# Kernel tuning notes

Measured on AMD Instinct MI355X. Metric: run time of the kernel, lower is better.

## Reference

```python
import jax, jax.numpy as jnp
import numpy as np

# Dimensions (see shape_source): 192x192 images, 10 MC samples, 4 classes (3 fg), batch 16
B, S, CLS, H, W = 16, 10, 4, 192, 192
FG = CLS - 1
FSCALE = 3   # neighbor-count kernel
CSCALE = 3   # constraint-reward kernel
K = float(CSCALE * CSCALE)


def setup_inputs() -> dict:
    key = jax.random.key(0)
    k1, k2 = jax.random.split(key)
    logits = jax.random.normal(k1, (B, CLS, H, W), dtype=jnp.float32)
    preds = jax.nn.softmax(logits, axis=1)          # per-pixel class probabilities
    samples = jax.random.randint(k2, (B, S, H, W), 0, CLS, dtype=jnp.int32)  # sampled label maps
    return {"preds": preds, "samples": samples}


def _conv_ones(x, ksize):
    # x: [N, H, W]; all-ones ksize x ksize conv, SAME padding (== pad (k-1)/2 in torch)
    kern = jnp.ones((1, 1, ksize, ksize), x.dtype)
    y = jax.lax.conv_general_dilated(x[:, None], kern, (1, 1), 'SAME')
    return y[:, 0]


def _dilate8(m):
    # 3x3 max-pool == one step of 8-connectivity dilation (skimage full connectivity)
    return jax.lax.reduce_window(m, 0.0, jax.lax.max, (3, 3), (1, 1), 'SAME')


def _flood(fg, seed):
    # connected component of fg containing flat index `seed` (8-connectivity),
    # equivalent to skimage.flood_fill from the seed followed by == new_value
    m0 = jnp.zeros(fg.size, fg.dtype).at[seed].set(1.0).reshape(fg.shape) * fg
    def cond(st):
        return st[1]
    def body(st):
        m, _ = st
        d = _dilate8(m) * fg
        return d, jnp.any(d != m)
    m, _ = jax.lax.while_loop(cond, body, (m0, jnp.array(True)))
    return m


def _connectivity_rewards(samples):
    # samples: [B, S, H, W] int class maps -> rewards [B, S, H, W]
    cls_ids = jnp.arange(1, CLS)
    fg = (samples[:, :, None] == cls_ids[None, None, :, None, None]).astype(jnp.float32)  # [B,S,FG,H,W]
    fgf = fg.reshape(-1, H, W)                     # [B*S*FG, H, W]
    nb = _conv_ones(fgf, FSCALE) * fgf             # foreground neighbor counts
    seeds = jnp.argmax(nb.reshape(nb.shape[0], -1), axis=1)  # seed = max-neighbor pixel (first max)
    comp = jax.vmap(_flood)(fgf, seeds)            # largest-seeded connected component
    fc = _conv_ones(comp, CSCALE) * comp           # F_fg_neigbors
    reward = fc / K                                # soft reward
    per_c = reward - (fgf - comp)                  # + isolation penalty: -(fg - fill_connect)
    return per_c.reshape(B, S, FG, H, W).sum(axis=2)


def reference(preds, samples):
    rewards = _connectivity_rewards(samples)       # [B,S,H,W], constant wrt preds
    # prob of the sampled class at each pixel: preds[b, samples[b,s,h,w], h, w]
    probs = jnp.take_along_axis(
        jnp.broadcast_to(preds[:, None], (B, S, CLS, H, W)),
        samples[:, :, None].astype(jnp.int32), axis=2)[:, :, 0]
    # REINFORCE-style constraint loss: maximize reward-weighted log-prob
    loss = -(jnp.log(probs + 1e-8) * rewards).mean()
    return loss
```

## Files before the change

kernel.cpp:

```cpp
#include <hip/hip_runtime.h>
#include <stdint.h>

#define BB 16
#define SS 10
#define CLSN 4
#define FGN 3
#define HH 192
#define WW 192
#define NPIX (HH * WW)
#define WPR 3
#define NWORDS (HH * WPR)
#define NTHREADS 1024
#define NWAVES 16
#define CHUNK (NWORDS / NWAVES)

typedef unsigned long long u64;

#define FAD(a, b, c, s, cy)            \
    do {                               \
        u64 t_ = (a) ^ (b);            \
        (s) = t_ ^ (c);                \
        (cy) = ((a) & (b)) | (t_ & (c)); \
    } while (0)

#define SMEAR3(u0, u1, u2, s0, s1, s2)                          \
    do {                                                        \
        (s0) = (u0) | ((u0) << 1) | ((u0) >> 1) | ((u1) << 63); \
        (s1) = (u1) | ((u1) << 1) | ((u0) >> 63) | ((u1) >> 1) | ((u2) << 63); \
        (s2) = (u2) | ((u2) << 1) | ((u1) >> 63) | ((u2) >> 1); \
    } while (0)

__device__ __forceinline__ void plane9(const u64* bd, int k,
                                       u64& P0, u64& P1, u64& P2, u64& P3, u64& mid)
{
    const int r = k / WPR;
    const int wc = k - r * WPR;
    u64 rows[3][3];
#pragma unroll
    for (int di = 0; di < 3; ++di) {
        int rr = r + di - 1;
#pragma unroll
        for (int dj = 0; dj < 3; ++dj) {
            int ww = wc + dj - 1;
            rows[di][dj] = (rr >= 0 && rr < HH && ww >= 0 && ww < WPR)
                           ? bd[rr * WPR + ww] : 0ULL;
        }
    }
    mid = rows[1][1];
    u64 in[9];
#pragma unroll
    for (int i = 0; i < 3; ++i) {
        u64 m = rows[i][1], lf = rows[i][0], rg = rows[i][2];
        in[3 * i + 0] = m;
        in[3 * i + 1] = (m << 1) | (lf >> 63);
        in[3 * i + 2] = (m >> 1) | (rg << 63);
    }
    u64 s0a, c0a, s0b, c0b, s0c, c0c, c0d, s1a, c1a, c1b;
    FAD(in[0], in[1], in[2], s0a, c0a);
    FAD(in[3], in[4], in[5], s0b, c0b);
    FAD(in[6], in[7], in[8], s0c, c0c);
    FAD(s0a, s0b, s0c, P0, c0d);
    FAD(c0a, c0b, c0c, s1a, c1a);
    P1 = s1a ^ c0d;
    c1b = s1a & c0d;
    P2 = c1a ^ c1b;
    P3 = c1a & c1b;
}

__global__ __launch_bounds__(NTHREADS) void cc_loss_kernel(
    const float* __restrict__ preds,
    const int* __restrict__ samples,
    double* __restrict__ acc)
{
    __shared__ u64 fgw[NWORDS];
    __shared__ u64 compB[NWORDS];
    __shared__ u64 pl[4][NWORDS];
    __shared__ unsigned int wkey[NWAVES];
    __shared__ double wsum[NWAVES];
    __shared__ unsigned int seedIdx;

    const int blk = blockIdx.x;
    const int c = 1 + blk / (BB * SS);
    const int pair = blk % (BB * SS);
    const int b = pair / SS;
    const int s = pair % SS;

    const int tid  = threadIdx.x;
    const int lane = tid & 63;
    const int wv   = tid >> 6;

    const int* smp = samples + (size_t)pair * NPIX;

    {
        const int base = wv * CHUNK;
        for (int i = 0; i < CHUNK; i += 6) {
            int v[6];
#pragma unroll
            for (int j = 0; j < 6; ++j)
                v[j] = smp[((base + i + j) << 6) + lane];
#pragma unroll
            for (int j = 0; j < 6; ++j) {
                u64 m = __ballot(v[j] == c);
                if (lane == 0) fgw[base + i + j] = m;
            }
        }
    }
    __syncthreads();

    {
        unsigned int bestkey = 0u;
        if (tid < NWORDS) {
            u64 P0, P1, P2, P3, mid;
            plane9(fgw, tid, P0, P1, P2, P3, mid);
            if (mid) {
                u64 cand = mid, t;
                unsigned v = 0;
                t = cand & P3; if (t) { cand = t; v |= 8u; }
                t = cand & P2; if (t) { cand = t; v |= 4u; }
                t = cand & P1; if (t) { cand = t; v |= 2u; }
                t = cand & P0; if (t) { cand = t; v |= 1u; }
                unsigned pix = ((unsigned)tid << 6) + (unsigned)(__ffsll(cand) - 1);
                bestkey = (v << 16) | (36863u - pix);
            }
        }
#pragma unroll
        for (int off = 32; off > 0; off >>= 1) {
            unsigned int o = (unsigned int)__shfl_xor((int)bestkey, off, 64);
            if (o > bestkey) bestkey = o;
        }
        if (lane == 0) wkey[wv] = bestkey;
    }
    __syncthreads();
    if (tid == 0) {
        unsigned int kk = 0u;
#pragma unroll
        for (int i = 0; i < NWAVES; ++i)
            if (wkey[i] > kk) kk = wkey[i];
        seedIdx = 36863u - (kk & 0xFFFFu);
    }
    __syncthreads();

    if (wv == 0) {
        const unsigned seed = seedIdx;
        u64 f[3][3], cc[3][3];
        const int rbase = 3 * lane;
#pragma unroll
        for (int j = 0; j < 3; ++j)
#pragma unroll
            for (int w = 0; w < 3; ++w) {
                f[j][w] = fgw[(rbase + j) * WPR + w];
                cc[j][w] = 0ULL;
            }
        {
            const int sr = seed / WW, sw = (seed % WW) >> 6, sb = seed & 63;
            if (sr / 3 == lane)
                cc[sr % 3][sw] = (1ULL << sb) & f[sr % 3][sw];
        }
        for (;;) {
            u64 bA0 = __shfl_up(cc[2][0], 1, 64);
            u64 bA1 = __shfl_up(cc[2][1], 1, 64);
            u64 bA2 = __shfl_up(cc[2][2], 1, 64);
            u64 tB0 = __shfl_down(cc[0][0], 1, 64);
            u64 tB1 = __shfl_down(cc[0][1], 1, 64);
            u64 tB2 = __shfl_down(cc[0][2], 1, 64);
            if (lane == 0)  { bA0 = bA1 = bA2 = 0ULL; }
            if (lane == 63) { tB0 = tB1 = tB2 = 0ULL; }

            u64 o00 = cc[0][0], o01 = cc[0][1], o02 = cc[0][2];
            u64 o10 = cc[1][0], o11 = cc[1][1], o12 = cc[1][2];
            u64 o20 = cc[2][0], o21 = cc[2][1], o22 = cc[2][2];

            u64 u0, u1, u2, s0, s1, s2;
            u0 = bA0 | cc[0][0] | cc[1][0]; u1 = bA1 | cc[0][1] | cc[1][1]; u2 = bA2 | cc[0][2] | cc[1][2];
            SMEAR3(u0, u1, u2, s0, s1, s2);
            cc[0][0] = s0 & f[0][0]; cc[0][1] = s1 & f[0][1]; cc[0][2] = s2 & f[0][2];

            u0 = cc[0][0] | cc[1][0] | cc[2][0]; u1 = cc[0][1] | cc[1][1] | cc[2][1]; u2 = cc[0][2] | cc[1][2] | cc[2][2];
            SMEAR3(u0, u1, u2, s0, s1, s2);
            cc[1][0] = s0 & f[1][0]; cc[1][1] = s1 & f[1][1]; cc[1][2] = s2 & f[1][2];

            u0 = cc[1][0] | cc[2][0] | tB0; u1 = cc[1][1] | cc[2][1] | tB1; u2 = cc[1][2] | cc[2][2] | tB2;
            SMEAR3(u0, u1, u2, s0, s1, s2);
            cc[2][0] = s0 & f[2][0]; cc[2][1] = s1 & f[2][1]; cc[2][2] = s2 & f[2][2];

            u0 = cc[0][0] | cc[1][0] | cc[2][0]; u1 = cc[0][1] | cc[1][1] | cc[2][1]; u2 = cc[0][2] | cc[1][2] | cc[2][2];
            SMEAR3(u0, u1, u2, s0, s1, s2);
            cc[1][0] = s0 & f[1][0]; cc[1][1] = s1 & f[1][1]; cc[1][2] = s2 & f[1][2];

            u0 = bA0 | cc[0][0] | cc[1][0]; u1 = bA1 | cc[0][1] | cc[1][1]; u2 = bA2 | cc[0][2] | cc[1][2];
            SMEAR3(u0, u1, u2, s0, s1, s2);
            cc[0][0] = s0 & f[0][0]; cc[0][1] = s1 & f[0][1]; cc[0][2] = s2 & f[0][2];

            u64 d = (cc[0][0] ^ o00) | (cc[0][1] ^ o01) | (cc[0][2] ^ o02)
                  | (cc[1][0] ^ o10) | (cc[1][1] ^ o11) | (cc[1][2] ^ o12)
                  | (cc[2][0] ^ o20) | (cc[2][1] ^ o21) | (cc[2][2] ^ o22);
            if (!__any(d != 0ULL)) break;
        }
#pragma unroll
        for (int j = 0; j < 3; ++j)
#pragma unroll
            for (int w = 0; w < 3; ++w)
                compB[(rbase + j) * WPR + w] = cc[j][w];
    }
    __syncthreads();

    if (tid < NWORDS) {
        u64 P0, P1, P2, P3, mid;
        plane9(compB, tid, P0, P1, P2, P3, mid);
        pl[0][tid] = P0; pl[1][tid] = P1; pl[2][tid] = P2; pl[3][tid] = P3;
    }
    __syncthreads();

    float facc = 0.0f;
    {
        const float* pp = preds + ((size_t)b * CLSN + c) * NPIX;
        const int dbase = wv * CHUNK;
        for (int i = 0; i < CHUNK; i += 4) {
            float pv[4];
            u64 fw[4], cw[4], q0[4], q1[4], q2[4], q3[4];
#pragma unroll
            for (int j = 0; j < 4; ++j) {
                int k = dbase + i + j;
                pv[j] = pp[(k << 6) + lane];
                fw[j] = fgw[k];
                cw[j] = compB[k];
                q0[j] = pl[0][k]; q1[j] = pl[1][k]; q2[j] = pl[2][k]; q3[j] = pl[3][k];
            }
#pragma unroll
            for (int j = 0; j < 4; ++j) {
                float lp = __logf(pv[j] + 1e-8f);
                int fgbit = (int)((fw[j] >> lane) & 1ULL);
                int cbit  = (int)((cw[j] >> lane) & 1ULL);
                int cnt = (int)((q0[j] >> lane) & 1ULL)
                        | ((int)((q1[j] >> lane) & 1ULL) << 1)
                        | ((int)((q2[j] >> lane) & 1ULL) << 2)
                        | ((int)((q3[j] >> lane) & 1ULL) << 3);
                float coef = cbit ? (float)cnt / 9.0f : (fgbit ? -1.0f : 0.0f);
                facc += coef * lp;
            }
        }
    }
#pragma unroll
    for (int off = 32; off > 0; off >>= 1)
        facc += __shfl_xor(facc, off, 64);
    if (lane == 0) wsum[wv] = (double)facc;
    __syncthreads();
    if (tid == 0) {
        double t = 0.0;
#pragma unroll
        for (int i = 0; i < NWAVES; ++i) t += wsum[i];
        atomicAdd(acc, t);
    }
}

__global__ void finalize_kernel(const double* __restrict__ acc, float* __restrict__ out)
{
    if (threadIdx.x == 0 && blockIdx.x == 0)
        out[0] = (float)(-acc[0] / (double)((long long)BB * SS * NPIX));
}

extern "C" void kernel_launch(void* const* d_in, const int* in_sizes, int n_in,
                              void* d_out, int out_size, void* d_ws, size_t ws_size,
                              hipStream_t stream)
{
    const float* preds   = (const float*)d_in[0];
    const int*   samples = (const int*)d_in[1];
    double* acc = (double*)d_ws;

    hipMemsetAsync(acc, 0, sizeof(double), stream);
    hipLaunchKernelGGL(cc_loss_kernel, dim3(BB * SS * FGN), dim3(NTHREADS), 0, stream,
                       preds, samples, acc);
    hipLaunchKernelGGL(finalize_kernel, dim3(1), dim3(64), 0, stream,
                       acc, (float*)d_out);
}
```

Baseline: 48.83 us.

## Fuse log-prob penalty into load pass, compute comp counts inline, halve block size

The preds load and the -(fg) log-prob term move into the first sample-loading pass, so each pixel's preds value is read and log-transformed alongside its label. The final pass then handles only words that hold component pixels, computing the 3x3 count planes inline. It drops the shared pl arrays and one barrier, and applies the coefficient cnt/9+1 to component pixels. Blocks shrink from 1024 to 512 threads, which lowers per-block shared memory and may raise occupancy, but the flood phase still uses a single wave and the first pass now does more work per wave.

```diff
diff --git a/kernel.cpp b/kernel.cpp
--- a/kernel.cpp
+++ b/kernel.cpp
@@ -10,9 +10,9 @@
 #define NPIX (HH * WW)
 #define WPR 3
 #define NWORDS (HH * WPR)
-#define NTHREADS 1024
-#define NWAVES 16
-#define CHUNK (NWORDS / NWAVES)
+#define NT 512
+#define NW 8
+#define CH (NWORDS / NW)
 
 typedef unsigned long long u64;
 
@@ -67,16 +67,15 @@
     P3 = c1a & c1b;
 }
 
-__global__ __launch_bounds__(NTHREADS) void cc_loss_kernel(
+__global__ __launch_bounds__(NT) void cc_loss_kernel(
     const float* __restrict__ preds,
     const int* __restrict__ samples,
     double* __restrict__ acc)
 {
     __shared__ u64 fgw[NWORDS];
     __shared__ u64 compB[NWORDS];
-    __shared__ u64 pl[4][NWORDS];
-    __shared__ unsigned int wkey[NWAVES];
-    __shared__ double wsum[NWAVES];
+    __shared__ unsigned int wkey[NW];
+    __shared__ double wsum[NW];
     __shared__ unsigned int seedIdx;
 
     const int blk = blockIdx.x;
@@ -90,18 +89,26 @@
     const int wv   = tid >> 6;
 
     const int* smp = samples + (size_t)pair * NPIX;
+    const float* pp = preds + ((size_t)b * CLSN + c) * NPIX;
+
+    float facc = 0.0f;
 
     {
-        const int base = wv * CHUNK;
-        for (int i = 0; i < CHUNK; i += 6) {
-            int v[6];
-#pragma unroll
-            for (int j = 0; j < 6; ++j)
-                v[j] = smp[((base + i + j) << 6) + lane];
+        const int base = wv * CH;
+        for (int i = 0; i < CH; i += 6) {
+            int v[6]; float pv[6];
+#pragma unroll
+            for (int j = 0; j < 6; ++j) {
+                int pix = ((base + i + j) << 6) + lane;
+                v[j]  = smp[pix];
+                pv[j] = pp[pix];
+            }
 #pragma unroll
             for (int j = 0; j < 6; ++j) {
                 u64 m = __ballot(v[j] == c);
                 if (lane == 0) fgw[base + i + j] = m;
+                float lp = __logf(pv[j] + 1e-8f);
+                facc -= (v[j] == c) ? lp : 0.0f;
             }
         }
     }
@@ -109,9 +116,9 @@
 
     {
         unsigned int bestkey = 0u;
-        if (tid < NWORDS) {
+        for (int k = tid; k < NWORDS; k += NT) {
             u64 P0, P1, P2, P3, mid;
-            plane9(fgw, tid, P0, P1, P2, P3, mid);
+            plane9(fgw, k, P0, P1, P2, P3, mid);
             if (mid) {
                 u64 cand = mid, t;
                 unsigned v = 0;
@@ -119,8 +126,9 @@
                 t = cand & P2; if (t) { cand = t; v |= 4u; }
                 t = cand & P1; if (t) { cand = t; v |= 2u; }
                 t = cand & P0; if (t) { cand = t; v |= 1u; }
-                unsigned pix = ((unsigned)tid << 6) + (unsigned)(__ffsll(cand) - 1);
-                bestkey = (v << 16) | (36863u - pix);
+                unsigned pix = ((unsigned)k << 6) + (unsigned)(__ffsll(cand) - 1);
+                unsigned key = (v << 16) | (36863u - pix);
+                if (key > bestkey) bestkey = key;
             }
         }
 #pragma unroll
@@ -134,7 +142,7 @@
     if (tid == 0) {
         unsigned int kk = 0u;
 #pragma unroll
-        for (int i = 0; i < NWAVES; ++i)
+        for (int i = 0; i < NW; ++i)
             if (wkey[i] > kk) kk = wkey[i];
         seedIdx = 36863u - (kk & 0xFFFFu);
     }
@@ -204,42 +212,24 @@
     }
     __syncthreads();
 
-    if (tid < NWORDS) {
-        u64 P0, P1, P2, P3, mid;
-        plane9(compB, tid, P0, P1, P2, P3, mid);
-        pl[0][tid] = P0; pl[1][tid] = P1; pl[2][tid] = P2; pl[3][tid] = P3;
-    }
-    __syncthreads();
-
-    float facc = 0.0f;
     {
-        const float* pp = preds + ((size_t)b * CLSN + c) * NPIX;
-        const int dbase = wv * CHUNK;
-        for (int i = 0; i < CHUNK; i += 4) {
-            float pv[4];
-            u64 fw[4], cw[4], q0[4], q1[4], q2[4], q3[4];
-#pragma unroll
-            for (int j = 0; j < 4; ++j) {
-                int k = dbase + i + j;
-                pv[j] = pp[(k << 6) + lane];
-                fw[j] = fgw[k];
-                cw[j] = compB[k];
-                q0[j] = pl[0][k]; q1[j] = pl[1][k]; q2[j] = pl[2][k]; q3[j] = pl[3][k];
-            }
-#pragma unroll
-            for (int j = 0; j < 4; ++j) {
-                float lp = __logf(pv[j] + 1e-8f);
-                int fgbit = (int)((fw[j] >> lane) & 1ULL);
-                int cbit  = (int)((cw[j] >> lane) & 1ULL);
-                int cnt = (int)((q0[j] >> lane) & 1ULL)
-                        | ((int)((q1[j] >> lane) & 1ULL) << 1)
-                        | ((int)((q2[j] >> lane) & 1ULL) << 2)
-                        | ((int)((q3[j] >> lane) & 1ULL) << 3);
-                float coef = cbit ? (float)cnt / 9.0f : (fgbit ? -1.0f : 0.0f);
-                facc += coef * lp;
-            }
-        }
-    }
+        const int base = wv * CH;
+        for (int k = base; k < base + CH; ++k) {
+            u64 cw = compB[k];
+            if (cw == 0ULL) continue;
+            u64 P0, P1, P2, P3, mid;
+            plane9(compB, k, P0, P1, P2, P3, mid);
+            if ((cw >> lane) & 1ULL) {
+                int cnt = (int)((P0 >> lane) & 1ULL)
+                        | ((int)((P1 >> lane) & 1ULL) << 1)
+                        | ((int)((P2 >> lane) & 1ULL) << 2)
+                        | ((int)((P3 >> lane) & 1ULL) << 3);
+                float lp = __logf(pp[(k << 6) + lane] + 1e-8f);
+                facc += ((float)cnt * (1.0f / 9.0f) + 1.0f) * lp;
+            }
+        }
+    }
+
 #pragma unroll
     for (int off = 32; off > 0; off >>= 1)
         facc += __shfl_xor(facc, off, 64);
@@ -248,7 +238,7 @@
     if (tid == 0) {
         double t = 0.0;
 #pragma unroll
-        for (int i = 0; i < NWAVES; ++i) t += wsum[i];
+        for (int i = 0; i < NW; ++i) t += wsum[i];
         atomicAdd(acc, t);
     }
 }
@@ -268,7 +258,7 @@
     double* acc = (double*)d_ws;
 
     hipMemsetAsync(acc, 0, sizeof(double), stream);
-    hipLaunchKernelGGL(cc_loss_kernel, dim3(BB * SS * FGN), dim3(NTHREADS), 0, stream,
+    hipLaunchKernelGGL(cc_loss_kernel, dim3(BB * SS * FGN), dim3(NT), 0, stream,
                        preds, samples, acc);
     hipLaunchKernelGGL(finalize_kernel, dim3(1), dim3(64), 0, stream,
                        acc, (float*)d_out);
```

Result: slower. 51.19 us (+4.8%).
